# Performance work log

Measured on AMD Instinct MI355X. Metric: run time of the kernel, lower is better.

The kernel has to match this reference:

```python
import jax, jax.numpy as jnp
import numpy as np

N_NODES = 100000
N_EDGES = 1600000
N_GRAPH = 100
IN_DIM = 64
LATENT = 128
STEPS = 2
MLP_LAYERS = 2
OUT_GLOBALS = 1
EPS = 1e-5  # haiku LayerNorm default


def setup_inputs() -> dict:
    key = jax.random.key(0)
    ks = jax.random.split(key, 8)
    nodes = jax.random.normal(ks[0], (N_NODES, IN_DIM), jnp.float32)
    senders = jax.random.randint(ks[1], (N_EDGES,), 0, N_NODES, jnp.int32)
    receivers = jax.random.randint(ks[2], (N_EDGES,), 0, N_NODES, jnp.int32)
    # 100 graphs of 1000 nodes each: jnp.repeat(arange(n_graph), n_node)
    graph_ids = (jnp.arange(N_NODES) // (N_NODES // N_GRAPH)).astype(jnp.int32)
    embed_w = jax.random.normal(ks[3], (IN_DIM, LATENT), jnp.float32) / np.sqrt(IN_DIM).astype(np.float32)
    embed_b = jnp.zeros((LATENT,), jnp.float32)
    mlp_w = jax.random.normal(ks[4], (STEPS, MLP_LAYERS, LATENT, LATENT), jnp.float32) / np.sqrt(LATENT).astype(np.float32)
    mlp_b = jnp.zeros((STEPS, MLP_LAYERS, LATENT), jnp.float32)
    ln_scale = jnp.ones((STEPS, LATENT), jnp.float32)
    ln_offset = jnp.zeros((STEPS, LATENT), jnp.float32)
    dec_w = jax.random.normal(ks[5], (LATENT, OUT_GLOBALS), jnp.float32) / np.sqrt(LATENT).astype(np.float32)
    dec_b = jnp.zeros((OUT_GLOBALS,), jnp.float32)
    return dict(nodes=nodes, senders=senders, receivers=receivers, graph_ids=graph_ids,
                embed_w=embed_w, embed_b=embed_b, mlp_w=mlp_w, mlp_b=mlp_b,
                ln_scale=ln_scale, ln_offset=ln_offset, dec_w=dec_w, dec_b=dec_b)


def _layernorm(x, scale, offset):
    mu = jnp.mean(x, axis=-1, keepdims=True)
    var = jnp.var(x, axis=-1, keepdims=True)
    return (x - mu) * jax.lax.rsqrt(var + EPS) * scale + offset


def reference(nodes, senders, receivers, graph_ids, embed_w, embed_b,
              mlp_w, mlp_b, ln_scale, ln_offset, dec_w, dec_b):
    n = nodes.shape[0]
    # jraph.GraphConvolution(add_self_edges=True, symmetric_normalization=True)
    self_loop = jnp.arange(n, dtype=senders.dtype)
    conv_s = jnp.concatenate([senders, self_loop])
    conv_r = jnp.concatenate([receivers, self_loop])
    ones_e = jnp.ones(conv_s.shape[0], jnp.float32)
    inv_sqrt_sdeg = jax.lax.rsqrt(jnp.maximum(jax.ops.segment_sum(ones_e, conv_s, n), 1.0))
    inv_sqrt_rdeg = jax.lax.rsqrt(jnp.maximum(jax.ops.segment_sum(ones_e, conv_r, n), 1.0))

    # embedder: hk.Linear on nodes
    h = nodes @ embed_w + embed_b

    for s in range(STEPS):
        # update_node_fn: MLP (dropout_rate=0 -> identity dropout)
        x = h
        for l in range(MLP_LAYERS):
            x = jax.nn.relu(x @ mlp_w[s, l] + mlp_b[s, l])
        # symmetric-normalized segment_sum aggregation with self-edges
        x = x * inv_sqrt_sdeg[:, None]
        x = jax.ops.segment_sum(x[conv_s], conv_r, num_segments=n)  # [n, LATENT]
        x = x * inv_sqrt_rdeg[:, None]
        h = x + h  # skip connection (add_graphs_tuples)
        h = _layernorm(h, ln_scale[s], ln_offset[s])

    # segment_mean pooling over graphs
    counts = jnp.maximum(jax.ops.segment_sum(jnp.ones(n, jnp.float32), graph_ids, N_GRAPH), 1.0)
    pooled = jax.ops.segment_sum(h, graph_ids, num_segments=N_GRAPH) / counts[:, None]
    # decoder: hk.Linear on pooled globals
    return pooled @ dec_w + dec_b  # [N_GRAPH, OUT_GLOBALS]
```

## Files before the change

### kernel.cpp

```cpp
#include <hip/hip_runtime.h>
#include <hip/hip_bf16.h>


#define N_NODES 100000
#define N_EDGES 1600000
#define N_GRAPH 100
#define NPG     1000
#define LATENT  128

#define NPART   8
#define PSIZE   (N_NODES / NPART)
#define NSLICE  32
#define ESLICE  (N_EDGES / NSLICE)

#define SCAN_CHUNK 2048
#define SCAN_NB    ((N_NODES + SCAN_CHUNK - 1) / SCAN_CHUNK)

#define PCHUNK  20
#define PCNODES (NPG / PCHUNK)

typedef __attribute__((ext_vector_type(8))) short short8;
typedef __attribute__((ext_vector_type(4))) float f32x4;

__device__ __forceinline__ unsigned short f2bf(float f) {
    union { float f; unsigned int u; } v; v.f = f;
    unsigned int r = v.u + 0x7fff + ((v.u >> 16) & 1);
    return (unsigned short)(r >> 16);
}
__device__ __forceinline__ float bf2f(unsigned short u) {
    union { unsigned int u; float f; } v; v.u = ((unsigned int)u) << 16;
    return v.f;
}

__global__ __launch_bounds__(1024) void k_hist2(const int* __restrict__ senders,
                                                const int* __restrict__ receivers,
                                                unsigned short* __restrict__ ps16,
                                                unsigned short* __restrict__ pr16) {
    __shared__ int cs[PSIZE];
    __shared__ int cr[PSIZE];
    int rg = blockIdx.x & (NPART - 1), sl = blockIdx.x >> 3;
    int lo = rg * PSIZE;
    for (int i = threadIdx.x; i < PSIZE; i += 1024) { cs[i] = 0; cr[i] = 0; }
    __syncthreads();
    int e0 = sl * ESLICE;
    for (int e = e0 + threadIdx.x; e < e0 + ESLICE; e += 1024) {
        int s = senders[e] - lo;
        if ((unsigned)s < PSIZE) atomicAdd(&cs[s], 1);
        int r = receivers[e] - lo;
        if ((unsigned)r < PSIZE) atomicAdd(&cr[r], 1);
    }
    __syncthreads();
    size_t base = (size_t)(rg * NSLICE + sl) * PSIZE;
    for (int i = threadIdx.x; i < PSIZE; i += 1024) {
        ps16[base + i] = (unsigned short)cs[i];
        pr16[base + i] = (unsigned short)cr[i];
    }
}

__global__ __launch_bounds__(256) void k_scan_slices(const unsigned short* __restrict__ ps16,
                                                     unsigned short* __restrict__ pr16,
                                                     int* __restrict__ deg_r,
                                                     float* __restrict__ inv_s,
                                                     float* __restrict__ inv_r) {
    int n = blockIdx.x * 256 + threadIdx.x;
    if (n >= N_NODES) return;
    int rg = n / PSIZE, i = n - rg * PSIZE;
    size_t base = (size_t)rg * NSLICE * PSIZE + i;
    int run = 0, ss = 0;
#pragma unroll 4
    for (int sl = 0; sl < NSLICE; sl++) {
        size_t idx = base + (size_t)sl * PSIZE;
        int v = pr16[idx];
        pr16[idx] = (unsigned short)run;
        run += v;
        ss += ps16[idx];
    }
    deg_r[n] = run;
    inv_r[n] = rsqrtf((float)(run + 1));
    inv_s[n] = rsqrtf((float)(ss + 1));
}

__global__ __launch_bounds__(256) void k_scan_block(const int* __restrict__ deg,
                                                    int* __restrict__ blocksums, int n) {
    int b = blockIdx.x, t = threadIdx.x;
    int base = b * SCAN_CHUNK + t * 8;
    int s = 0;
#pragma unroll
    for (int j = 0; j < 8; j++) { int i = base + j; if (i < n) s += deg[i]; }
    __shared__ int wsum[4];
#pragma unroll
    for (int off = 32; off > 0; off >>= 1) s += __shfl_down(s, off, 64);
    if ((t & 63) == 0) wsum[t >> 6] = s;
    __syncthreads();
    if (t == 0) blocksums[b] = wsum[0] + wsum[1] + wsum[2] + wsum[3];
}

__global__ __launch_bounds__(64) void k_scan_top(int* __restrict__ blocksums, int nb) {
    int t = threadIdx.x;
    int v = (t < nb) ? blocksums[t] : 0;
    int inc = v;
#pragma unroll
    for (int off = 1; off < 64; off <<= 1) {
        int u = __shfl_up(inc, off, 64);
        if (t >= off) inc += u;
    }
    if (t < nb) blocksums[t] = inc - v;
}

__global__ __launch_bounds__(256) void k_scan_apply(const int* __restrict__ deg,
                                                    const int* __restrict__ blockoffs,
                                                    int* __restrict__ row_start, int n) {
    int b = blockIdx.x, t = threadIdx.x;
    int base = b * SCAN_CHUNK + t * 8;
    int v[8]; int tsum = 0;
#pragma unroll
    for (int j = 0; j < 8; j++) { int i = base + j; v[j] = (i < n) ? deg[i] : 0; tsum += v[j]; }
    __shared__ int wtot[4];
    int inc = tsum;
#pragma unroll
    for (int off = 1; off < 64; off <<= 1) {
        int u = __shfl_up(inc, off, 64);
        if ((t & 63) >= off) inc += u;
    }
    if ((t & 63) == 63) wtot[t >> 6] = inc;
    __syncthreads();
    int wbase = 0;
    for (int w = 0; w < (t >> 6); w++) wbase += wtot[w];
    int running = blockoffs[b] + wbase + (inc - tsum);
#pragma unroll
    for (int j = 0; j < 8; j++) {
        int i = base + j;
        if (i < n) {
            row_start[i] = running;
            running += v[j];
            if (i == n - 1) row_start[n] = running;
        }
    }
}

__global__ __launch_bounds__(1024) void k_fill2(const int* __restrict__ senders,
                                                const int* __restrict__ receivers,
                                                const unsigned short* __restrict__ pr16,
                                                const int* __restrict__ row_start,
                                                int* __restrict__ edge_src) {
    __shared__ int bs[PSIZE];
    int rg = blockIdx.x & (NPART - 1), sl = blockIdx.x >> 3;
    int lo = rg * PSIZE;
    const unsigned short* base = pr16 + (size_t)(rg * NSLICE + sl) * PSIZE;
    for (int i = threadIdx.x; i < PSIZE; i += 1024)
        bs[i] = row_start[lo + i] + (int)base[i];
    __syncthreads();
    int e0 = sl * ESLICE;
    for (int e = e0 + threadIdx.x; e < e0 + ESLICE; e += 1024) {
        int r = receivers[e] - lo;
        if ((unsigned)r < PSIZE) {
            int pos = atomicAdd(&bs[r], 1);
            edge_src[pos] = senders[e];
        }
    }
}

__global__ void k_wprep(const float* __restrict__ embed_w, const float* __restrict__ mlp_w,
                        unsigned short* __restrict__ hi, unsigned short* __restrict__ lo) {
    int t = blockIdx.x * 256 + threadIdx.x;
    if (t >= 8192 + 4 * 16384) return;
    const float* src; int local;
    if (t < 8192) { src = embed_w; local = t; }
    else { int m = t - 8192; src = mlp_w + (size_t)(m >> 14) * 16384; local = m & 16383; }
    int j = local & 7, lane = (local >> 3) & 63, tn = (local >> 9) & 7, kc = local >> 12;
    int k = kc * 32 + ((lane >> 4) << 3) + j;
    int n = tn * 16 + (lane & 15);
    float wv = src[k * 128 + n];
    unsigned short h = f2bf(wv);
    float rem = wv - bf2f(h);
    hi[t] = h; lo[t] = f2bf(rem);
}

__global__ __launch_bounds__(256) void k_embed_mlp(
    const float* __restrict__ A,
    const unsigned short* __restrict__ wehi, const unsigned short* __restrict__ welo,
    const float* __restrict__ eb,
    const unsigned short* __restrict__ w0hi, const unsigned short* __restrict__ w0lo,
    const unsigned short* __restrict__ w1hi, const unsigned short* __restrict__ w1lo,
    const float* __restrict__ b0, const float* __restrict__ b1,
    const float* __restrict__ inv_s,
    unsigned short* __restrict__ h16, unsigned short* __restrict__ x16, int M)
{
    __shared__ __align__(16) unsigned short t0[4][32][136];
    int t = threadIdx.x, w = t >> 6, L = t & 63;
    int m0 = blockIdx.x * 128 + w * 32;
    int lr = L & 15, lk = (L >> 4) * 8, lq = (L >> 4) * 4;

    float ebv[8], b0v[8], b1v[8];
#pragma unroll
    for (int tn = 0; tn < 8; tn++) {
        ebv[tn] = eb[tn * 16 + lr];
        b0v[tn] = b0[tn * 16 + lr];
        b1v[tn] = b1[tn * 16 + lr];
    }

    f32x4 acc[2][8];
#pragma unroll
    for (int bd = 0; bd < 2; bd++)
#pragma unroll
        for (int tn = 0; tn < 8; tn++) acc[bd][tn] = (f32x4){0.f, 0.f, 0.f, 0.f};
#pragma unroll
    for (int kc = 0; kc < 2; kc++) {
        short8 a[2];
#pragma unroll
        for (int bd = 0; bd < 2; bd++) {
            int grow = m0 + bd * 16 + lr; if (grow >= M) grow = M - 1;
            const float* rp = A + (size_t)grow * 64 + kc * 32 + lk;
            float4 v0 = *(const float4*)rp;
            float4 v1 = *(const float4*)(rp + 4);
            short8 pk;
            pk[0] = (short)f2bf(v0.x); pk[1] = (short)f2bf(v0.y);
            pk[2] = (short)f2bf(v0.z); pk[3] = (short)f2bf(v0.w);
            pk[4] = (short)f2bf(v1.x); pk[5] = (short)f2bf(v1.y);
            pk[6] = (short)f2bf(v1.z); pk[7] = (short)f2bf(v1.w);
            a[bd] = pk;
        }
#pragma unroll
        for (int tn = 0; tn < 8; tn++) {
            size_t fo = (size_t)(((kc * 8 + tn) * 64 + L)) * 8;
            short8 bh = *(const short8*)(wehi + fo);
            short8 bl = *(const short8*)(welo + fo);
#pragma unroll
            for (int bd = 0; bd < 2; bd++) {
                acc[bd][tn] = __builtin_amdgcn_mfma_f32_16x16x32_bf16(a[bd], bh, acc[bd][tn], 0, 0, 0);
                acc[bd][tn] = __builtin_amdgcn_mfma_f32_16x16x32_bf16(a[bd], bl, acc[bd][tn], 0, 0, 0);
            }
        }
    }
#pragma unroll
    for (int bd = 0; bd < 2; bd++)
#pragma unroll
        for (int tn = 0; tn < 8; tn++)
#pragma unroll
            for (int r = 0; r < 4; r++)
                t0[w][bd * 16 + lq + r][tn * 16 + lr] = f2bf(acc[bd][tn][r] + ebv[tn]);
#pragma unroll
    for (int q = 0; q < 8; q++) {
        int s = q * 64 + L;
        int row = s >> 4, c0 = (s & 15) * 8;
        int grow = m0 + row;
        if (grow < M)
            *(short8*)(h16 + (size_t)grow * 128 + c0) = *(const short8*)&t0[w][row][c0];
    }

#pragma unroll
    for (int bd = 0; bd < 2; bd++)
#pragma unroll
        for (int tn = 0; tn < 8; tn++) acc[bd][tn] = (f32x4){0.f, 0.f, 0.f, 0.f};
#pragma unroll
    for (int kc = 0; kc < 4; kc++) {
        short8 a[2];
#pragma unroll
        for (int bd = 0; bd < 2; bd++)
            a[bd] = *(const short8*)&t0[w][bd * 16 + lr][kc * 32 + lk];
#pragma unroll
        for (int tn = 0; tn < 8; tn++) {
            size_t fo = (size_t)(((kc * 8 + tn) * 64 + L)) * 8;
            short8 bh = *(const short8*)(w0hi + fo);
            short8 bl = *(const short8*)(w0lo + fo);
#pragma unroll
            for (int bd = 0; bd < 2; bd++) {
                acc[bd][tn] = __builtin_amdgcn_mfma_f32_16x16x32_bf16(a[bd], bh, acc[bd][tn], 0, 0, 0);
                acc[bd][tn] = __builtin_amdgcn_mfma_f32_16x16x32_bf16(a[bd], bl, acc[bd][tn], 0, 0, 0);
            }
        }
    }
#pragma unroll
    for (int bd = 0; bd < 2; bd++)
#pragma unroll
        for (int tn = 0; tn < 8; tn++)
#pragma unroll
            for (int r = 0; r < 4; r++)
                t0[w][bd * 16 + lq + r][tn * 16 + lr] = f2bf(fmaxf(acc[bd][tn][r] + b0v[tn], 0.f));

#pragma unroll
    for (int bd = 0; bd < 2; bd++)
#pragma unroll
        for (int tn = 0; tn < 8; tn++) acc[bd][tn] = (f32x4){0.f, 0.f, 0.f, 0.f};
#pragma unroll
    for (int kc = 0; kc < 4; kc++) {
        short8 a[2];
#pragma unroll
        for (int bd = 0; bd < 2; bd++)
            a[bd] = *(const short8*)&t0[w][bd * 16 + lr][kc * 32 + lk];
#pragma unroll
        for (int tn = 0; tn < 8; tn++) {
            size_t fo = (size_t)(((kc * 8 + tn) * 64 + L)) * 8;
            short8 bh = *(const short8*)(w1hi + fo);
            short8 bl = *(const short8*)(w1lo + fo);
#pragma unroll
            for (int bd = 0; bd < 2; bd++) {
                acc[bd][tn] = __builtin_amdgcn_mfma_f32_16x16x32_bf16(a[bd], bh, acc[bd][tn], 0, 0, 0);
                acc[bd][tn] = __builtin_amdgcn_mfma_f32_16x16x32_bf16(a[bd], bl, acc[bd][tn], 0, 0, 0);
            }
        }
    }
    float invs[2][4];
#pragma unroll
    for (int bd = 0; bd < 2; bd++)
#pragma unroll
        for (int r = 0; r < 4; r++) {
            int grow = m0 + bd * 16 + lq + r; if (grow >= M) grow = M - 1;
            invs[bd][r] = inv_s[grow];
        }
#pragma unroll
    for (int bd = 0; bd < 2; bd++)
#pragma unroll
        for (int tn = 0; tn < 8; tn++)
#pragma unroll
            for (int r = 0; r < 4; r++)
                t0[w][bd * 16 + lq + r][tn * 16 + lr] =
                    f2bf(fmaxf(acc[bd][tn][r] + b1v[tn], 0.f) * invs[bd][r]);
#pragma unroll
    for (int q = 0; q < 8; q++) {
        int s = q * 64 + L;
        int row = s >> 4, c0 = (s & 15) * 8;
        int grow = m0 + row;
        if (grow < M)
            *(short8*)(x16 + (size_t)grow * 128 + c0) = *(const short8*)&t0[w][row][c0];
    }
}

__global__ __launch_bounds__(256) void k_mlp(
    const unsigned short* __restrict__ A16, const unsigned short* __restrict__ w0hi,
    const unsigned short* __restrict__ w0lo, const unsigned short* __restrict__ w1hi,
    const unsigned short* __restrict__ w1lo, const float* __restrict__ b0,
    const float* __restrict__ b1, const float* __restrict__ inv_s,
    unsigned short* __restrict__ x16, int M)
{
    __shared__ __align__(16) unsigned short t1[4][32][136];
    int t = threadIdx.x, w = t >> 6, L = t & 63;
    int m0 = blockIdx.x * 128 + w * 32;
    int lr = L & 15, lk = (L >> 4) * 8, lq = (L >> 4) * 4;

    float b0v[8], b1v[8];
#pragma unroll
    for (int tn = 0; tn < 8; tn++) { b0v[tn] = b0[tn * 16 + lr]; b1v[tn] = b1[tn * 16 + lr]; }

    f32x4 acc[2][8];
#pragma unroll
    for (int bd = 0; bd < 2; bd++)
#pragma unroll
        for (int tn = 0; tn < 8; tn++) acc[bd][tn] = (f32x4){0.f, 0.f, 0.f, 0.f};

#pragma unroll
    for (int kc = 0; kc < 4; kc++) {
        short8 a[2];
#pragma unroll
        for (int bd = 0; bd < 2; bd++) {
            int grow = m0 + bd * 16 + lr; if (grow >= M) grow = M - 1;
            a[bd] = *(const short8*)(A16 + (size_t)grow * 128 + kc * 32 + lk);
        }
#pragma unroll
        for (int tn = 0; tn < 8; tn++) {
            size_t fo = (size_t)(((kc * 8 + tn) * 64 + L)) * 8;
            short8 bh = *(const short8*)(w0hi + fo);
            short8 bl = *(const short8*)(w0lo + fo);
#pragma unroll
            for (int bd = 0; bd < 2; bd++) {
                acc[bd][tn] = __builtin_amdgcn_mfma_f32_16x16x32_bf16(a[bd], bh, acc[bd][tn], 0, 0, 0);
                acc[bd][tn] = __builtin_amdgcn_mfma_f32_16x16x32_bf16(a[bd], bl, acc[bd][tn], 0, 0, 0);
            }
        }
    }
#pragma unroll
    for (int bd = 0; bd < 2; bd++)
#pragma unroll
        for (int tn = 0; tn < 8; tn++)
#pragma unroll
            for (int r = 0; r < 4; r++)
                t1[w][bd * 16 + lq + r][tn * 16 + lr] = f2bf(fmaxf(acc[bd][tn][r] + b0v[tn], 0.f));

    f32x4 acc2[2][8];
#pragma unroll
    for (int bd = 0; bd < 2; bd++)
#pragma unroll
        for (int tn = 0; tn < 8; tn++) acc2[bd][tn] = (f32x4){0.f, 0.f, 0.f, 0.f};
#pragma unroll
    for (int kc = 0; kc < 4; kc++) {
        short8 a[2];
#pragma unroll
        for (int bd = 0; bd < 2; bd++)
            a[bd] = *(const short8*)&t1[w][bd * 16 + lr][kc * 32 + lk];
#pragma unroll
        for (int tn = 0; tn < 8; tn++) {
            size_t fo = (size_t)(((kc * 8 + tn) * 64 + L)) * 8;
            short8 bh = *(const short8*)(w1hi + fo);
            short8 bl = *(const short8*)(w1lo + fo);
#pragma unroll
            for (int bd = 0; bd < 2; bd++) {
                acc2[bd][tn] = __builtin_amdgcn_mfma_f32_16x16x32_bf16(a[bd], bh, acc2[bd][tn], 0, 0, 0);
                acc2[bd][tn] = __builtin_amdgcn_mfma_f32_16x16x32_bf16(a[bd], bl, acc2[bd][tn], 0, 0, 0);
            }
        }
    }
    float invs[2][4];
#pragma unroll
    for (int bd = 0; bd < 2; bd++)
#pragma unroll
        for (int r = 0; r < 4; r++) {
            int grow = m0 + bd * 16 + lq + r; if (grow >= M) grow = M - 1;
            invs[bd][r] = inv_s[grow];
        }
#pragma unroll
    for (int bd = 0; bd < 2; bd++)
#pragma unroll
        for (int tn = 0; tn < 8; tn++)
#pragma unroll
            for (int r = 0; r < 4; r++)
                t1[w][bd * 16 + lq + r][tn * 16 + lr] =
                    f2bf(fmaxf(acc2[bd][tn][r] + b1v[tn], 0.f) * invs[bd][r]);
#pragma unroll
    for (int q = 0; q < 8; q++) {
        int s = q * 64 + L;
        int row = s >> 4, c0 = (s & 15) * 8;
        int grow = m0 + row;
        if (grow < M)
            *(short8*)(x16 + (size_t)grow * 128 + c0) = *(const short8*)&t1[w][row][c0];
    }
}

__global__ __launch_bounds__(256) void k_agg_ln(
    const unsigned short* __restrict__ x16, const int* __restrict__ row_start,
    const int* __restrict__ edge_src, const float* __restrict__ inv_r,
    const float* __restrict__ ln_scale, const float* __restrict__ ln_offset,
    unsigned short* __restrict__ h16)
{
    int node = __builtin_amdgcn_readfirstlane(blockIdx.x * 4 + (threadIdx.x >> 6));
    int L = threadIdx.x & 63;
    const unsigned int* x32 = (const unsigned int*)x16;
    const unsigned int* h32 = (const unsigned int*)h16;

    unsigned int su = x32[(size_t)node * 64 + L];
    float2 acc;
    acc.x = __uint_as_float(su << 16);
    acc.y = __uint_as_float(su & 0xffff0000u);

    int beg = row_start[node], end = row_start[node + 1];
    int j = beg;
    for (; j + 8 <= end; j += 8) {
        unsigned int u[8];
#pragma unroll
        for (int q = 0; q < 8; q++) u[q] = x32[(size_t)edge_src[j + q] * 64 + L];
#pragma unroll
        for (int q = 0; q < 8; q++) {
            acc.x += __uint_as_float(u[q] << 16);
            acc.y += __uint_as_float(u[q] & 0xffff0000u);
        }
    }
    for (; j < end; j++) {
        unsigned int u0 = x32[(size_t)edge_src[j] * 64 + L];
        acc.x += __uint_as_float(u0 << 16);
        acc.y += __uint_as_float(u0 & 0xffff0000u);
    }

    float ir = inv_r[node];
    unsigned int hu = h32[(size_t)node * 64 + L];
    float y0 = acc.x * ir + __uint_as_float(hu << 16);
    float y1 = acc.y * ir + __uint_as_float(hu & 0xffff0000u);

    float s1 = y0 + y1, s2 = y0 * y0 + y1 * y1;
#pragma unroll
    for (int off = 32; off > 0; off >>= 1) {
        s1 += __shfl_xor(s1, off, 64);
        s2 += __shfl_xor(s2, off, 64);
    }
    float mu = s1 * (1.f / 128.f);
    float var = fmaxf(s2 * (1.f / 128.f) - mu * mu, 0.f);
    float rstd = rsqrtf(var + 1e-5f);
    float2 sc = *(const float2*)&ln_scale[L * 2];
    float2 of = *(const float2*)&ln_offset[L * 2];
    float ox = (y0 - mu) * rstd * sc.x + of.x;
    float oy = (y1 - mu) * rstd * sc.y + of.y;
    ((unsigned int*)h16)[(size_t)node * 64 + L] =
        (unsigned int)f2bf(ox) | ((unsigned int)f2bf(oy) << 16);
}

__global__ __launch_bounds__(256) void k_pool1(const unsigned short* __restrict__ h16,
                                               float* __restrict__ partial) {
    int b = blockIdx.x;
    int g = b / PCHUNK, c = b % PCHUNK;
    int t = threadIdx.x, col = t & 127, half = t >> 7;
    const unsigned short* hg = h16 + ((size_t)g * NPG + (size_t)c * PCNODES) * 128;
    float acc = 0.f;
    for (int i = half; i < PCNODES; i += 2) acc += bf2f(hg[(size_t)i * 128 + col]);
    __shared__ float red[256];
    red[t] = acc;
    __syncthreads();
    if (half == 0) partial[(size_t)b * 128 + col] = red[col] + red[col + 128];
}

__global__ __launch_bounds__(128) void k_pool2(const float* __restrict__ partial,
                                               const float* __restrict__ dec_w,
                                               const float* __restrict__ dec_b,
                                               float* __restrict__ out) {
    int g = blockIdx.x, col = threadIdx.x;
    const float* pg = partial + (size_t)g * PCHUNK * 128;
    float s = 0.f;
#pragma unroll
    for (int c = 0; c < PCHUNK; c++) s += pg[c * 128 + col];
    s = s * (1.f / (float)NPG) * dec_w[col];
    __shared__ float ws[2];
#pragma unroll
    for (int off = 32; off > 0; off >>= 1) s += __shfl_down(s, off, 64);
    if ((col & 63) == 0) ws[col >> 6] = s;
    __syncthreads();
    if (col == 0) out[g] = ws[0] + ws[1] + dec_b[0];
}

extern "C" void kernel_launch(void* const* d_in, const int* in_sizes, int n_in,
                              void* d_out, int out_size, void* d_ws, size_t ws_size,
                              hipStream_t stream) {
    (void)in_sizes; (void)n_in; (void)out_size; (void)ws_size;
    const float* nodes     = (const float*)d_in[0];
    const int*   senders   = (const int*)d_in[1];
    const int*   receivers = (const int*)d_in[2];
    const float* embed_w   = (const float*)d_in[4];
    const float* embed_b   = (const float*)d_in[5];
    const float* mlp_w     = (const float*)d_in[6];
    const float* mlp_b     = (const float*)d_in[7];
    const float* ln_scale  = (const float*)d_in[8];
    const float* ln_offset = (const float*)d_in[9];
    const float* dec_w     = (const float*)d_in[10];
    const float* dec_b     = (const float*)d_in[11];
    float* out = (float*)d_out;

    const int N = N_NODES;
    const int WF_TOTAL = 8192 + 4 * 16384;
    const int PART_TOTAL = NPART * NSLICE * PSIZE;

    char* p = (char*)d_ws;
    auto alloc = [&](size_t bytes) -> void* {
        void* r = (void*)p;
        p += (bytes + 255) & ~(size_t)255;
        return r;
    };
    unsigned short* h16      = (unsigned short*)alloc((size_t)N * 128 * 2);
    unsigned short* x16      = (unsigned short*)alloc((size_t)N * 128 * 2);
    int*            edge_src = (int*)alloc((size_t)N_EDGES * 4);
    unsigned short* ps16     = (unsigned short*)alloc((size_t)PART_TOTAL * 2);
    unsigned short* pr16     = (unsigned short*)alloc((size_t)PART_TOTAL * 2);
    int*            deg_r    = (int*)alloc((size_t)N * 4);
    float*          inv_s    = (float*)alloc((size_t)N * 4);
    float*          inv_r    = (float*)alloc((size_t)N * 4);
    int*            row_start= (int*)alloc((size_t)(N + 1) * 4);
    int*            blocksums= (int*)alloc((size_t)SCAN_NB * 4);
    unsigned short* wfhi     = (unsigned short*)alloc((size_t)WF_TOTAL * 2);
    unsigned short* wflo     = (unsigned short*)alloc((size_t)WF_TOTAL * 2);
    float*          poolpart = (float*)alloc((size_t)N_GRAPH * PCHUNK * 128 * 4);

    k_wprep<<<(WF_TOTAL + 255) / 256, 256, 0, stream>>>(embed_w, mlp_w, wfhi, wflo);

    k_hist2<<<NPART * NSLICE, 1024, 0, stream>>>(senders, receivers, ps16, pr16);
    k_scan_slices<<<(N + 255) / 256, 256, 0, stream>>>(ps16, pr16, deg_r, inv_s, inv_r);
    k_scan_block<<<SCAN_NB, 256, 0, stream>>>(deg_r, blocksums, N);
    k_scan_top<<<1, 64, 0, stream>>>(blocksums, SCAN_NB);
    k_scan_apply<<<SCAN_NB, 256, 0, stream>>>(deg_r, blocksums, row_start, N);
    k_fill2<<<NPART * NSLICE, 1024, 0, stream>>>(senders, receivers, pr16, row_start, edge_src);

    int mblocks = (N + 127) / 128;
    const unsigned short* wehi = wfhi, *welo = wflo;
    const unsigned short* w0hi[2] = { wfhi + 8192,             wfhi + 8192 + 2 * 16384 };
    const unsigned short* w0lo[2] = { wflo + 8192,             wflo + 8192 + 2 * 16384 };
    const unsigned short* w1hi[2] = { wfhi + 8192 + 16384,     wfhi + 8192 + 3 * 16384 };
    const unsigned short* w1lo[2] = { wflo + 8192 + 16384,     wflo + 8192 + 3 * 16384 };

    k_embed_mlp<<<mblocks, 256, 0, stream>>>(nodes, wehi, welo, embed_b,
                                             w0hi[0], w0lo[0], w1hi[0], w1lo[0],
                                             mlp_b, mlp_b + 128, inv_s, h16, x16, N);
    k_agg_ln<<<N / 4, 256, 0, stream>>>(x16, row_start, edge_src, inv_r,
                                        ln_scale, ln_offset, h16);
    k_mlp<<<mblocks, 256, 0, stream>>>(h16, w0hi[1], w0lo[1], w1hi[1], w1lo[1],
                                       mlp_b + 256, mlp_b + 384, inv_s, x16, N);
    k_agg_ln<<<N / 4, 256, 0, stream>>>(x16, row_start, edge_src, inv_r,
                                        ln_scale + 128, ln_offset + 128, h16);

    k_pool1<<<N_GRAPH * PCHUNK, 256, 0, stream>>>(h16, poolpart);
    k_pool2<<<N_GRAPH, 128, 0, stream>>>(poolpart, dec_w, dec_b, out);
}
```

Baseline: 423.3 us.

## Split per-node aggregation across two waves and pack histogram counters to 16-bit

The aggregation plus LayerNorm kernel now gives each node two wavefronts. Each wave gathers half of the node's incoming edges, and the two partial sums are combined through shared memory before normalization. This doubles the memory-level parallelism available for the irregular gathers, at the cost of a block barrier, more waves, and redundant LayerNorm math in the second wave. Separately, the degree histogram packs two 16-bit counters per shared-memory word. That allows 4 node partitions instead of 8, with 64 edge slices. The edge arrays are therefore re-read fewer times, but the fill kernel now needs a larger shared buffer per block.

```diff
diff --git a/kernel.cpp b/kernel.cpp
--- a/kernel.cpp
+++ b/kernel.cpp
@@ -8,9 +8,9 @@
 #define NPG     1000
 #define LATENT  128
 
-#define NPART   8
+#define NPART   4
 #define PSIZE   (N_NODES / NPART)
-#define NSLICE  32
+#define NSLICE  64
 #define ESLICE  (N_EDGES / NSLICE)
 
 #define SCAN_CHUNK 2048
@@ -36,24 +36,24 @@
                                                 const int* __restrict__ receivers,
                                                 unsigned short* __restrict__ ps16,
                                                 unsigned short* __restrict__ pr16) {
-    __shared__ int cs[PSIZE];
-    __shared__ int cr[PSIZE];
-    int rg = blockIdx.x & (NPART - 1), sl = blockIdx.x >> 3;
+    __shared__ unsigned int cs[PSIZE / 2];
+    __shared__ unsigned int cr[PSIZE / 2];
+    int rg = blockIdx.x & (NPART - 1), sl = blockIdx.x >> 2;
     int lo = rg * PSIZE;
-    for (int i = threadIdx.x; i < PSIZE; i += 1024) { cs[i] = 0; cr[i] = 0; }
+    for (int i = threadIdx.x; i < PSIZE / 2; i += 1024) { cs[i] = 0; cr[i] = 0; }
     __syncthreads();
     int e0 = sl * ESLICE;
     for (int e = e0 + threadIdx.x; e < e0 + ESLICE; e += 1024) {
         int s = senders[e] - lo;
-        if ((unsigned)s < PSIZE) atomicAdd(&cs[s], 1);
+        if ((unsigned)s < PSIZE) atomicAdd(&cs[s >> 1], 1u << ((s & 1) * 16));
         int r = receivers[e] - lo;
-        if ((unsigned)r < PSIZE) atomicAdd(&cr[r], 1);
+        if ((unsigned)r < PSIZE) atomicAdd(&cr[r >> 1], 1u << ((r & 1) * 16));
     }
     __syncthreads();
     size_t base = (size_t)(rg * NSLICE + sl) * PSIZE;
     for (int i = threadIdx.x; i < PSIZE; i += 1024) {
-        ps16[base + i] = (unsigned short)cs[i];
-        pr16[base + i] = (unsigned short)cr[i];
+        ps16[base + i] = (unsigned short)((cs[i >> 1] >> ((i & 1) * 16)) & 0xffff);
+        pr16[base + i] = (unsigned short)((cr[i >> 1] >> ((i & 1) * 16)) & 0xffff);
     }
 }
 
@@ -144,7 +144,7 @@
                                                 const int* __restrict__ row_start,
                                                 int* __restrict__ edge_src) {
     __shared__ int bs[PSIZE];
-    int rg = blockIdx.x & (NPART - 1), sl = blockIdx.x >> 3;
+    int rg = blockIdx.x & (NPART - 1), sl = blockIdx.x >> 2;
     int lo = rg * PSIZE;
     const unsigned short* base = pr16 + (size_t)(rg * NSLICE + sl) * PSIZE;
     for (int i = threadIdx.x; i < PSIZE; i += 1024)
@@ -431,19 +431,28 @@
     const float* __restrict__ ln_scale, const float* __restrict__ ln_offset,
     unsigned short* __restrict__ h16)
 {
-    int node = __builtin_amdgcn_readfirstlane(blockIdx.x * 4 + (threadIdx.x >> 6));
-    int L = threadIdx.x & 63;
+    __shared__ float2 part[4][64];
+    int w = threadIdx.x >> 6, L = threadIdx.x & 63;
+    int node = __builtin_amdgcn_readfirstlane(blockIdx.x * 2 + (w >> 1));
+    int half = w & 1;
     const unsigned int* x32 = (const unsigned int*)x16;
     const unsigned int* h32 = (const unsigned int*)h16;
 
-    unsigned int su = x32[(size_t)node * 64 + L];
     float2 acc;
-    acc.x = __uint_as_float(su << 16);
-    acc.y = __uint_as_float(su & 0xffff0000u);
+    if (half == 0) {
+        unsigned int su = x32[(size_t)node * 64 + L];
+        acc.x = __uint_as_float(su << 16);
+        acc.y = __uint_as_float(su & 0xffff0000u);
+    } else {
+        acc.x = 0.f; acc.y = 0.f;
+    }
 
     int beg = row_start[node], end = row_start[node + 1];
-    int j = beg;
-    for (; j + 8 <= end; j += 8) {
+    int mid = beg + ((end - beg) >> 1);
+    int jb = half ? mid : beg;
+    int je = half ? end : mid;
+    int j = jb;
+    for (; j + 8 <= je; j += 8) {
         unsigned int u[8];
 #pragma unroll
         for (int q = 0; q < 8; q++) u[q] = x32[(size_t)edge_src[j + q] * 64 + L];
@@ -453,11 +462,16 @@
             acc.y += __uint_as_float(u[q] & 0xffff0000u);
         }
     }
-    for (; j < end; j++) {
+    for (; j < je; j++) {
         unsigned int u0 = x32[(size_t)edge_src[j] * 64 + L];
         acc.x += __uint_as_float(u0 << 16);
         acc.y += __uint_as_float(u0 & 0xffff0000u);
     }
+
+    part[w][L] = acc;
+    __syncthreads();
+    float2 o = part[w ^ 1][L];
+    acc.x += o.x; acc.y += o.y;
 
     float ir = inv_r[node];
     unsigned int hu = h32[(size_t)node * 64 + L];
@@ -477,8 +491,9 @@
     float2 of = *(const float2*)&ln_offset[L * 2];
     float ox = (y0 - mu) * rstd * sc.x + of.x;
     float oy = (y1 - mu) * rstd * sc.y + of.y;
-    ((unsigned int*)h16)[(size_t)node * 64 + L] =
-        (unsigned int)f2bf(ox) | ((unsigned int)f2bf(oy) << 16);
+    if (half == 0)
+        ((unsigned int*)h16)[(size_t)node * 64 + L] =
+            (unsigned int)f2bf(ox) | ((unsigned int)f2bf(oy) << 16);
 }
 
 __global__ __launch_bounds__(256) void k_pool1(const unsigned short* __restrict__ h16,
@@ -532,7 +547,7 @@
 
     const int N = N_NODES;
     const int WF_TOTAL = 8192 + 4 * 16384;
-    const int PART_TOTAL = NPART * NSLICE * PSIZE;
+    const size_t PART_TOTAL = (size_t)NPART * NSLICE * PSIZE;
 
     char* p = (char*)d_ws;
     auto alloc = [&](size_t bytes) -> void* {
@@ -543,8 +558,8 @@
     unsigned short* h16      = (unsigned short*)alloc((size_t)N * 128 * 2);
     unsigned short* x16      = (unsigned short*)alloc((size_t)N * 128 * 2);
     int*            edge_src = (int*)alloc((size_t)N_EDGES * 4);
-    unsigned short* ps16     = (unsigned short*)alloc((size_t)PART_TOTAL * 2);
-    unsigned short* pr16     = (unsigned short*)alloc((size_t)PART_TOTAL * 2);
+    unsigned short* ps16     = (unsigned short*)alloc(PART_TOTAL * 2);
+    unsigned short* pr16     = (unsigned short*)alloc(PART_TOTAL * 2);
     int*            deg_r    = (int*)alloc((size_t)N * 4);
     float*          inv_s    = (float*)alloc((size_t)N * 4);
     float*          inv_r    = (float*)alloc((size_t)N * 4);
@@ -573,11 +588,11 @@
     k_embed_mlp<<<mblocks, 256, 0, stream>>>(nodes, wehi, welo, embed_b,
                                              w0hi[0], w0lo[0], w1hi[0], w1lo[0],
                                              mlp_b, mlp_b + 128, inv_s, h16, x16, N);
-    k_agg_ln<<<N / 4, 256, 0, stream>>>(x16, row_start, edge_src, inv_r,
+    k_agg_ln<<<N / 2, 256, 0, stream>>>(x16, row_start, edge_src, inv_r,
                                         ln_scale, ln_offset, h16);
     k_mlp<<<mblocks, 256, 0, stream>>>(h16, w0hi[1], w0lo[1], w1hi[1], w1lo[1],
                                        mlp_b + 256, mlp_b + 384, inv_s, x16, N);
-    k_agg_ln<<<N / 4, 256, 0, stream>>>(x16, row_start, edge_src, inv_r,
+    k_agg_ln<<<N / 2, 256, 0, stream>>>(x16, row_start, edge_src, inv_r,
                                         ln_scale + 128, ln_offset + 128, h16);
 
     k_pool1<<<N_GRAPH * PCHUNK, 256, 0, stream>>>(h16, poolpart);
```

Result: slower. 513.5 us (+21.3%).
